# Optimization experiments

Measured on AMD Instinct MI355X. Metric: run time of the kernel, lower is better.

The kernel has to match this reference:

```python
import jax, jax.numpy as jnp
import numpy as np

K = 10
SLOPE = 0.2
FEATS = [3, 64, 128, 256, 512, 1024]
MLP = [1024, 128, 64, 1]
B, N = 8, 2048


def setup_inputs() -> dict:
    key = jax.random.key(0)
    keys = jax.random.split(key, 32)
    inp = {"x": jax.random.normal(keys[0], (B, N, 3), dtype=jnp.float32)}
    ki = 1
    for i in range(5):
        fin, fout = 2 * FEATS[i], FEATS[i + 1]
        s = 1.0 / np.sqrt(fin)
        inp[f"w{i}"] = jax.random.uniform(keys[ki], (fin, fout), jnp.float32, -s, s); ki += 1
        inp[f"b{i}"] = jax.random.uniform(keys[ki], (fout,), jnp.float32, -s, s); ki += 1
    for i in range(3):
        fin, fout = MLP[i], MLP[i + 1]
        s = 1.0 / np.sqrt(fin)
        inp[f"m{i}w"] = jax.random.uniform(keys[ki], (fin, fout), jnp.float32, -s, s); ki += 1
        inp[f"m{i}b"] = jax.random.uniform(keys[ki], (fout,), jnp.float32, -s, s); ki += 1
    return inp


def _knn_idx(xb):
    # xb: [N, F]; squared euclidean distances, self included (dist 0)
    sq = jnp.sum(xb * xb, axis=-1)
    d2 = sq[:, None] + sq[None, :] - 2.0 * (xb @ xb.T)
    _, idx = jax.lax.top_k(-d2, K)  # [N, K] nearest (incl. self)
    return idx


def _edge_conv(x, W, b):
    # x: [B, N, F] -> [B, N, Fout]
    fin = x.shape[-1]
    W1, W2 = W[:fin], W[fin:]  # split concat([x_i, x_j - x_i]) @ W
    idx = jax.vmap(_knn_idx)(x)  # [B, N, K]
    x_j = jax.vmap(lambda xb, ib: xb[ib])(x, idx)  # [B, N, K, F]
    h_center = x @ W1 + b  # [B, N, Fout]
    diff = x_j - x[:, :, None, :]
    h = h_center[:, :, None, :] + jnp.einsum('bnkf,fo->bnko', diff, W2)
    h = jnp.where(h > 0, h, SLOPE * h)  # LeakyReLU(0.2)
    return jnp.max(h, axis=2)  # max aggregation over neighbors


def reference(x, w0, b0, w1, b1, w2, b2, w3, b3, w4, b4,
              m0w, m0b, m1w, m1b, m2w, m2b):
    ws = [(w0, b0), (w1, b1), (w2, b2), (w3, b3), (w4, b4)]
    h = x
    for W, b in ws:
        h = _edge_conv(h, W, b)
    g = jnp.max(h, axis=1)  # MaxPool1d(kernel=2048) -> global max over points: [B, 1024]
    g = g @ m0w + m0b
    g = g @ m1w + m1b
    g = g @ m2w + m2b
    return g  # [B, 1]
```

## Files before the change

kernel.cpp:

```cpp
#include <hip/hip_runtime.h>
#include <hip/hip_bf16.h>
#include <math.h>

#define BB 8
#define NN 2048
#define KK 10
#define BN (BB * NN)
#define HC 1024
#define GCH 64

typedef __attribute__((ext_vector_type(8))) short bf16x8;
typedef __attribute__((ext_vector_type(4))) float f32x4;

__device__ inline unsigned short f2bf(float f) {
    unsigned int u = __float_as_uint(f);
    unsigned int r = u + 0x7fffu + ((u >> 16) & 1u);
    return (unsigned short)(r >> 16);
}
__device__ inline float bf2f(unsigned short h) {
    return __uint_as_float((unsigned int)h << 16);
}

__device__ __forceinline__ void async16(const void* g, void* l) {
    __builtin_amdgcn_global_load_lds(
        (const __attribute__((address_space(1))) void*)g,
        (__attribute__((address_space(3))) void*)l, 16, 0, 0);
}

__global__ void xsplit3_kernel(const float* __restrict__ x,
                               unsigned short* __restrict__ hi,
                               unsigned short* __restrict__ lo,
                               float* __restrict__ sq) {
    int row = blockIdx.x * blockDim.x + threadIdx.x;
    if (row >= BN) return;
    unsigned short hbuf[32], lbuf[32];
#pragma unroll
    for (int f = 0; f < 32; ++f) { hbuf[f] = 0; lbuf[f] = 0; }
    float s = 0.f;
#pragma unroll
    for (int f = 0; f < 3; ++f) {
        float v = x[(size_t)row * 3 + f];
        s += v * v;
        unsigned short h = f2bf(v);
        hbuf[f] = h;
        lbuf[f] = f2bf(v - bf2f(h));
    }
    sq[row] = s;
#pragma unroll
    for (int f = 0; f < 32; f += 8) {
        *(uint4*)&hi[(size_t)row * 32 + f] = *(uint4*)&hbuf[f];
        *(uint4*)&lo[(size_t)row * 32 + f] = *(uint4*)&lbuf[f];
    }
}

__global__ void wsplit_all_kernel(const float* __restrict__ w0, const float* __restrict__ w1,
                                  const float* __restrict__ w2, const float* __restrict__ w3,
                                  const float* __restrict__ w4, unsigned short* __restrict__ WTall) {
    const int fins[5]  = {3, 64, 128, 256, 512};
    const int fpads[5] = {32, 64, 128, 256, 512};
    const int fouts[5] = {64, 128, 256, 512, 1024};
    const int eoff[6]  = {0, 4096, 20480, 86016, 348160, 1396736};
    const int woff[5]  = {0, 8192, 40960, 172032, 696320};
    int i = blockIdx.x * blockDim.x + threadIdx.x;
    if (i >= 1396736) return;
    int l;
    if (i < eoff[1]) l = 0; else if (i < eoff[2]) l = 1;
    else if (i < eoff[3]) l = 2; else if (i < eoff[4]) l = 3; else l = 4;
    int e = i - eoff[l];
    const float* w = (l == 0) ? w0 : (l == 1) ? w1 : (l == 2) ? w2 : (l == 3) ? w3 : w4;
    int fin = fins[l], fpad = fpads[l], fout = fouts[l];
    unsigned short* WT = WTall + woff[l];
    int op = e % (2 * fout);
    int f = e / (2 * fout);
    float v = 0.f;
    if (f < fin) {
        if (op < fout) v = w[(size_t)f * fout + op] - w[(size_t)(fin + f) * fout + op];
        else v = w[(size_t)(fin + f) * fout + (op - fout)];
    }
    unsigned short h = f2bf(v);
    unsigned short lo = f2bf(v - bf2f(h));
    WT[(size_t)op * (2 * fpad) + f] = h;
    WT[(size_t)op * (2 * fpad) + fpad + f] = lo;
}

__global__ __launch_bounds__(256) void knn_gram_kernel(
        const unsigned short* __restrict__ xh, const unsigned short* __restrict__ xl,
        const float* __restrict__ sq, float* __restrict__ d2a,
        float* __restrict__ d2b, int F) {
    int b = blockIdx.y;
    int t = blockIdx.x, ti = 0;
    while (t >= 16 - ti) { t -= 16 - ti; ti++; }
    int tj = ti + t;
    int row0 = ti * 128;
    int col0 = tj * 128;
    const unsigned short* xhb = xh + (size_t)b * NN * F;
    const unsigned short* xlb = xl + (size_t)b * NN * F;
    const float* sqb = sq + (size_t)b * NN;

    __shared__ __align__(16) unsigned char smem_raw[33024];
    unsigned short* Ah = (unsigned short*)smem_raw;
    unsigned short* Al = Ah + 128 * 32;
    unsigned short* Bh = Al + 128 * 32;
    unsigned short* Bl = Bh + 128 * 32;
    float* LT = (float*)smem_raw;

    int tid = threadIdx.x;
    int lane = tid & 63;
    int wave = tid >> 6;
    int wr = (wave >> 1) * 64, wc = (wave & 1) * 64;
    int l15 = lane & 15, kq = lane >> 4;
    int rsub = lane >> 2;
    int csub = (((lane & 3) ^ ((lane >> 3) & 3))) * 8;
    int kqs = (kq ^ ((l15 >> 1) & 3)) * 8;

    f32x4 acc[4][4];
#pragma unroll
    for (int mt = 0; mt < 4; ++mt)
#pragma unroll
        for (int nt = 0; nt < 4; ++nt) acc[mt][nt] = (f32x4){0.f, 0.f, 0.f, 0.f};

    for (int kc = 0; kc < F; kc += 32) {
        __syncthreads();
#pragma unroll
        for (int j = 0; j < 2; ++j) {
            int row = wave * 32 + j * 16 + rsub;
            int dsto = wave * 1024 + j * 512;
            async16(xhb + (size_t)(row0 + row) * F + kc + csub, Ah + dsto);
            async16(xlb + (size_t)(row0 + row) * F + kc + csub, Al + dsto);
            async16(xhb + (size_t)(col0 + row) * F + kc + csub, Bh + dsto);
            async16(xlb + (size_t)(col0 + row) * F + kc + csub, Bl + dsto);
        }
        __syncthreads();
        bf16x8 bh[4], bl[4];
#pragma unroll
        for (int t4 = 0; t4 < 4; ++t4) {
            bh[t4] = *(const bf16x8*)&Bh[(wc + t4 * 16 + l15) * 32 + kqs];
            bl[t4] = *(const bf16x8*)&Bl[(wc + t4 * 16 + l15) * 32 + kqs];
        }
#pragma unroll
        for (int mt = 0; mt < 4; ++mt) {
            bf16x8 ah = *(const bf16x8*)&Ah[(wr + mt * 16 + l15) * 32 + kqs];
            bf16x8 al = *(const bf16x8*)&Al[(wr + mt * 16 + l15) * 32 + kqs];
#pragma unroll
            for (int nt = 0; nt < 4; ++nt) {
                acc[mt][nt] = __builtin_amdgcn_mfma_f32_16x16x32_bf16(ah, bh[nt], acc[mt][nt], 0, 0, 0);
                acc[mt][nt] = __builtin_amdgcn_mfma_f32_16x16x32_bf16(al, bh[nt], acc[mt][nt], 0, 0, 0);
                acc[mt][nt] = __builtin_amdgcn_mfma_f32_16x16x32_bf16(ah, bl[nt], acc[mt][nt], 0, 0, 0);
            }
        }
    }
    {
        float* dst = (col0 < HC) ? d2a : d2b;
        int lc0 = col0 & (HC - 1);
#pragma unroll
        for (int mt = 0; mt < 4; ++mt) {
            int rbase = row0 + wr + mt * 16 + kq * 4;
#pragma unroll
            for (int nt = 0; nt < 4; ++nt) {
                int cc = wc + nt * 16 + l15;
                float sqc = sqb[col0 + cc];
#pragma unroll
                for (int r = 0; r < 4; ++r) {
                    float v = (sqb[rbase + r] + sqc) - 2.f * acc[mt][nt][r];
                    acc[mt][nt][r] = v;
                    dst[((size_t)b * NN + rbase + r) * HC + lc0 + cc] = v;
                }
            }
        }
    }
    if (ti != tj) {
        float* mdst = (row0 < HC) ? d2a : d2b;
        int mc0 = row0 & (HC - 1);
#pragma unroll
        for (int h = 0; h < 2; ++h) {
            __syncthreads();
            if ((wave & 1) == h) {
#pragma unroll
                for (int mt = 0; mt < 4; ++mt)
#pragma unroll
                    for (int nt = 0; nt < 4; ++nt)
#pragma unroll
                        for (int r = 0; r < 4; ++r)
                            LT[(nt * 16 + l15) * 129 + (wr + mt * 16 + kq * 4 + r)] =
                                acc[mt][nt][r];
            }
            __syncthreads();
#pragma unroll
            for (int it = 0; it < 8; ++it) {
                int v = tid + it * 256;
                int lr = v >> 5, c4 = v & 31;
                float4 val;
                val.x = LT[lr * 129 + c4 * 4];
                val.y = LT[lr * 129 + c4 * 4 + 1];
                val.z = LT[lr * 129 + c4 * 4 + 2];
                val.w = LT[lr * 129 + c4 * 4 + 3];
                *(float4*)&mdst[((size_t)b * NN + col0 + h * 64 + lr) * HC + mc0 + c4 * 4] = val;
            }
        }
    }
}

__global__ __launch_bounds__(256) void knn_select_kernel(
        const float* __restrict__ d2a, const float* __restrict__ d2b,
        int* __restrict__ idx) {
    int row = blockIdx.x * 4 + (threadIdx.x >> 6);
    int lane = threadIdx.x & 63;
    const float* ra = d2a + (size_t)row * HC;
    const float* rb = d2b + (size_t)row * HC;

    float4 v[8];
#pragma unroll
    for (int it = 0; it < 4; ++it) {
        v[it]     = *(const float4*)&ra[it * 256 + lane * 4];
        v[it + 4] = *(const float4*)&rb[it * 256 + lane * 4];
    }

    float bestd[KK];
    int besti[KK];
#pragma unroll
    for (int k = 0; k < KK; ++k) { bestd[k] = INFINITY; besti[k] = 0x7fffffff; }

#pragma unroll
    for (int it = 0; it < 8; ++it) {
        int cbase = ((it < 4) ? (it * 256) : (HC + (it - 4) * 256)) + lane * 4;
        float dv[4] = {v[it].x, v[it].y, v[it].z, v[it].w};
#pragma unroll
        for (int s4 = 0; s4 < 4; ++s4) {
            float d = dv[s4];
            if (d < bestd[KK - 1]) {
                bestd[KK - 1] = d;
                besti[KK - 1] = cbase + s4;
#pragma unroll
                for (int s = KK - 1; s > 0; --s) {
                    if (bestd[s] < bestd[s - 1]) {
                        float td = bestd[s]; bestd[s] = bestd[s - 1]; bestd[s - 1] = td;
                        int ti = besti[s]; besti[s] = besti[s - 1]; besti[s - 1] = ti;
                    }
                }
            }
        }
    }

    int h = 0;
    int mywin = 0;
    for (int s = 0; s < KK; ++s) {
        float dd = (h < KK) ? bestd[h] : INFINITY;
        int ii = (h < KK) ? besti[h] : 0x7fffffff;
        float d0 = dd; int i0 = ii;
#pragma unroll
        for (int off = 32; off > 0; off >>= 1) {
            float od = __shfl_xor(dd, off);
            int oi = __shfl_xor(ii, off);
            if (od < dd || (od == dd && oi < ii)) { dd = od; ii = oi; }
        }
        if (lane == s) mywin = ii;
        if (h < KK && i0 == ii && d0 == dd) h++;
    }
    if (lane < KK) idx[(size_t)row * KK + lane] = mywin;
}

__global__ __launch_bounds__(256) void gemm2_mfma_kernel(
        const unsigned short* __restrict__ XSh, const unsigned short* __restrict__ XSl,
        const unsigned short* __restrict__ WT, const float* __restrict__ bias,
        float* __restrict__ Aout, float* __restrict__ Tout, int fin, int fout) {
    int m0 = blockIdx.x * 128;
    int n0 = blockIdx.y * 128;
    __shared__ __align__(16) unsigned short AsB[4 * 128 * 32];
    unsigned short* Ah = AsB;
    unsigned short* Al = Ah + 128 * 32;
    unsigned short* Bh = Al + 128 * 32;
    unsigned short* Bl = Bh + 128 * 32;

    int tid = threadIdx.x;
    int lane = tid & 63;
    int wave = tid >> 6;
    int wr = (wave >> 1) * 64, wc = (wave & 1) * 64;
    int l15 = lane & 15, kq = lane >> 4;
    int rsub = lane >> 2;
    int csub = (((lane & 3) ^ ((lane >> 3) & 3))) * 8;
    int kqs = (kq ^ ((l15 >> 1) & 3)) * 8;
    int w2f = 2 * fin;

    f32x4 acc[4][4];
#pragma unroll
    for (int mt = 0; mt < 4; ++mt)
#pragma unroll
        for (int nt = 0; nt < 4; ++nt) acc[mt][nt] = (f32x4){0.f, 0.f, 0.f, 0.f};

    for (int kc = 0; kc < fin; kc += 32) {
        __syncthreads();
#pragma unroll
        for (int j = 0; j < 2; ++j) {
            int row = wave * 32 + j * 16 + rsub;
            int dsto = wave * 1024 + j * 512;
            async16(XSh + (size_t)(m0 + row) * fin + kc + csub, Ah + dsto);
            async16(XSl + (size_t)(m0 + row) * fin + kc + csub, Al + dsto);
            async16(WT + (size_t)(n0 + row) * w2f + kc + csub, Bh + dsto);
            async16(WT + (size_t)(n0 + row) * w2f + fin + kc + csub, Bl + dsto);
        }
        __syncthreads();
        bf16x8 bh[4], bl[4];
#pragma unroll
        for (int t = 0; t < 4; ++t) {
            bh[t] = *(const bf16x8*)&Bh[(wc + t * 16 + l15) * 32 + kqs];
            bl[t] = *(const bf16x8*)&Bl[(wc + t * 16 + l15) * 32 + kqs];
        }
#pragma unroll
        for (int mt = 0; mt < 4; ++mt) {
            bf16x8 ah = *(const bf16x8*)&Ah[(wr + mt * 16 + l15) * 32 + kqs];
            bf16x8 al = *(const bf16x8*)&Al[(wr + mt * 16 + l15) * 32 + kqs];
#pragma unroll
            for (int nt = 0; nt < 4; ++nt) {
                acc[mt][nt] = __builtin_amdgcn_mfma_f32_16x16x32_bf16(ah, bh[nt], acc[mt][nt], 0, 0, 0);
                acc[mt][nt] = __builtin_amdgcn_mfma_f32_16x16x32_bf16(al, bh[nt], acc[mt][nt], 0, 0, 0);
                acc[mt][nt] = __builtin_amdgcn_mfma_f32_16x16x32_bf16(ah, bl[nt], acc[mt][nt], 0, 0, 0);
            }
        }
    }
#pragma unroll
    for (int mt = 0; mt < 4; ++mt) {
        int mbase = m0 + wr + mt * 16 + kq * 4;
#pragma unroll
        for (int nt = 0; nt < 4; ++nt) {
            int oc = n0 + wc + nt * 16 + l15;
            f32x4 c = acc[mt][nt];
            if (oc < fout) {
                float bv = bias[oc];
#pragma unroll
                for (int r = 0; r < 4; ++r)
                    Aout[(size_t)(mbase + r) * fout + oc] = c[r] + bv;
            } else {
                int o2 = oc - fout;
#pragma unroll
                for (int r = 0; r < 4; ++r)
                    Tout[(size_t)(mbase + r) * fout + o2] = c[r];
            }
        }
    }
}

__global__ __launch_bounds__(256) void gathermax_fused_kernel(
        const float* __restrict__ A, const float* __restrict__ T,
        const int* __restrict__ idx, unsigned short* __restrict__ hi,
        unsigned short* __restrict__ lo, float* __restrict__ sq, int shift) {
    int b = blockIdx.y;
    int wave = threadIdx.x >> 6;
    int lane = threadIdx.x & 63;
    int pnl = blockIdx.x * 4 + wave;
    int pn = (b << 11) + pnl;
    int fout = 1 << shift;
    int nf4 = fout >> 2;
    const float* Tb = T + ((size_t)b << 11) * fout;
    const int* ip = idx + (size_t)pn * KK;
    int j[KK];
#pragma unroll
    for (int k = 0; k < KK; ++k) j[k] = ip[k];

    float s = 0.f;
    for (int f4 = lane; f4 < nf4; f4 += 64) {
        int o = f4 * 4;
        float4 m = {-INFINITY, -INFINITY, -INFINITY, -INFINITY};
#pragma unroll
        for (int k = 0; k < KK; ++k) {
            float4 t = *(const float4*)&Tb[(size_t)j[k] * fout + o];
            m.x = fmaxf(m.x, t.x); m.y = fmaxf(m.y, t.y);
            m.z = fmaxf(m.z, t.z); m.w = fmaxf(m.w, t.w);
        }
        float4 a = *(const float4*)&A[(size_t)pn * fout + o];
        float h4[4];
        h4[0] = a.x + m.x; h4[1] = a.y + m.y; h4[2] = a.z + m.z; h4[3] = a.w + m.w;
        uint2 uh, ul;
        unsigned short hs[4], ls[4];
#pragma unroll
        for (int q = 0; q < 4; ++q) {
            float h = h4[q] > 0.f ? h4[q] : 0.2f * h4[q];
            s += h * h;
            unsigned short hh = f2bf(h);
            hs[q] = hh;
            ls[q] = f2bf(h - bf2f(hh));
        }
        uh.x = (unsigned)hs[0] | ((unsigned)hs[1] << 16);
        uh.y = (unsigned)hs[2] | ((unsigned)hs[3] << 16);
        ul.x = (unsigned)ls[0] | ((unsigned)ls[1] << 16);
        ul.y = (unsigned)ls[2] | ((unsigned)ls[3] << 16);
        *(uint2*)&hi[(size_t)pn * fout + o] = uh;
        *(uint2*)&lo[(size_t)pn * fout + o] = ul;
    }
#pragma unroll
    for (int off = 32; off > 0; off >>= 1) s += __shfl_down(s, off);
    if (lane == 0) sq[pn] = s;
}

__global__ __launch_bounds__(256) void gathermax_gmax_kernel(
        const float* __restrict__ A, const float* __restrict__ T,
        const int* __restrict__ idx, float* __restrict__ gp) {
    int chunk = blockIdx.x;
    int b = blockIdx.y;
    int o = threadIdx.x * 4;
    const float* Tb = T + ((size_t)b << 11) * 1024;
    float4 gm = {-INFINITY, -INFINITY, -INFINITY, -INFINITY};
    for (int p = 0; p < NN / GCH; ++p) {
        int pnl = chunk * (NN / GCH) + p;
        int pn = (b << 11) + pnl;
        const int* ip = idx + (size_t)pn * KK;
        float4 m = {-INFINITY, -INFINITY, -INFINITY, -INFINITY};
#pragma unroll
        for (int k = 0; k < KK; ++k) {
            int j = ip[k];
            float4 t = *(const float4*)&Tb[(size_t)j * 1024 + o];
            m.x = fmaxf(m.x, t.x); m.y = fmaxf(m.y, t.y);
            m.z = fmaxf(m.z, t.z); m.w = fmaxf(m.w, t.w);
        }
        float4 a = *(const float4*)&A[(size_t)pn * 1024 + o];
        float4 h;
        h.x = a.x + m.x; h.y = a.y + m.y; h.z = a.z + m.z; h.w = a.w + m.w;
        h.x = h.x > 0.f ? h.x : 0.2f * h.x;
        h.y = h.y > 0.f ? h.y : 0.2f * h.y;
        h.z = h.z > 0.f ? h.z : 0.2f * h.z;
        h.w = h.w > 0.f ? h.w : 0.2f * h.w;
        gm.x = fmaxf(gm.x, h.x); gm.y = fmaxf(gm.y, h.y);
        gm.z = fmaxf(gm.z, h.z); gm.w = fmaxf(gm.w, h.w);
    }
    *(float4*)&gp[((size_t)chunk * BB + b) * 1024 + o] = gm;
}

__global__ void gmax2_kernel(const float* __restrict__ gp, float* __restrict__ g) {
    int i = blockIdx.x * 256 + threadIdx.x;
    int b = i >> 10, o = i & 1023;
    float m = -INFINITY;
    for (int c = 0; c < GCH; ++c) m = fmaxf(m, gp[((size_t)c * BB + b) * 1024 + o]);
    g[(size_t)b * 1024 + o] = m;
}

__global__ __launch_bounds__(256) void mlp1_kernel(
        const float* __restrict__ g, const float* __restrict__ m0w,
        const float* __restrict__ m0b, float* __restrict__ H1) {
    int wid = blockIdx.x * 4 + (threadIdx.x >> 6);
    int lane = threadIdx.x & 63;
    int b = wid >> 7, t = wid & 127;
    float s = 0.f;
    for (int f = lane; f < 1024; f += 64)
        s += g[(size_t)b * 1024 + f] * m0w[(size_t)f * 128 + t];
#pragma unroll
    for (int off = 32; off > 0; off >>= 1) s += __shfl_down(s, off);
    if (lane == 0) H1[(size_t)b * 128 + t] = s + m0b[t];
}

__global__ __launch_bounds__(256) void mlp2_kernel(
        const float* __restrict__ H1, const float* __restrict__ m1w,
        const float* __restrict__ m1b, float* __restrict__ H2) {
    int wid = blockIdx.x * 4 + (threadIdx.x >> 6);
    int lane = threadIdx.x & 63;
    int b = wid >> 6, t = wid & 63;
    float s = 0.f;
    for (int f = lane; f < 128; f += 64)
        s += H1[(size_t)b * 128 + f] * m1w[(size_t)f * 64 + t];
#pragma unroll
    for (int off = 32; off > 0; off >>= 1) s += __shfl_down(s, off);
    if (lane == 0) H2[(size_t)b * 64 + t] = s + m1b[t];
}

__global__ __launch_bounds__(256) void mlp3_kernel(
        const float* __restrict__ H2, const float* __restrict__ m2w,
        const float* __restrict__ m2b, float* __restrict__ out) {
    int b = blockIdx.x * 4 + (threadIdx.x >> 6);
    int lane = threadIdx.x & 63;
    if (b >= BB) return;
    float s = H2[(size_t)b * 64 + lane] * m2w[lane];
#pragma unroll
    for (int off = 32; off > 0; off >>= 1) s += __shfl_down(s, off);
    if (lane == 0) out[b] = s + m2b[0];
}

extern "C" void kernel_launch(void* const* d_in, const int* in_sizes, int n_in,
                              void* d_out, int out_size, void* d_ws, size_t ws_size,
                              hipStream_t stream) {
    const float* x0 = (const float*)d_in[0];
    const float* w[5], * bi[5];
    for (int i = 0; i < 5; ++i) { w[i] = (const float*)d_in[1 + 2 * i]; bi[i] = (const float*)d_in[2 + 2 * i]; }
    const float* m0w = (const float*)d_in[11]; const float* m0b = (const float*)d_in[12];
    const float* m1w = (const float*)d_in[13]; const float* m1b = (const float*)d_in[14];
    const float* m2w = (const float*)d_in[15]; const float* m2b = (const float*)d_in[16];

    const int fouts[5] = {64, 128, 256, 512, 1024};
    const int shifts[5] = {6, 7, 8, 9, 10};
    const int woff[5] = {0, 8192, 40960, 172032, 696320};
    const size_t WTALL = 2793472;

    float* X0 = (float*)d_ws;
    float* X1 = X0 + (size_t)BN * 1024;
    float* T  = X1 + (size_t)BN * 1024;
    float* SQ = T  + (size_t)BN * 1024;
    int*   IDX = (int*)(SQ + BN);
    unsigned short* XSh = (unsigned short*)(IDX + (size_t)BN * KK);
    unsigned short* XSl = XSh + (size_t)BN * 512;
    unsigned short* WTall = XSl + (size_t)BN * 512;
    float* GP = (float*)(WTall + WTALL);
    float* G  = GP + (size_t)GCH * BB * 1024;
    float* H1 = G + (size_t)BB * 1024;
    float* H2 = H1 + (size_t)BB * 128;
    float* bufs[2] = {X0, X1};

    xsplit3_kernel<<<(BN + 255) / 256, 256, 0, stream>>>(x0, XSh, XSl, SQ);
    wsplit_all_kernel<<<(1396736 + 255) / 256, 256, 0, stream>>>(w[0], w[1], w[2], w[3], w[4], WTall);

    int fin = 3;
    for (int l = 0; l < 5; ++l) {
        int fout = fouts[l];
        float* nxt = bufs[l & 1];
        int Fg = (l == 0) ? 32 : fin;

        dim3 gg2(136, BB);
        knn_gram_kernel<<<gg2, 256, 0, stream>>>(XSh, XSl, SQ, T, nxt, Fg);
        knn_select_kernel<<<BN / 4, 256, 0, stream>>>(T, nxt, IDX);

        dim3 gg(BN / 128, (2 * fout) / 128);
        gemm2_mfma_kernel<<<gg, 256, 0, stream>>>(XSh, XSl, WTall + woff[l], bi[l], nxt, T, Fg, fout);

        if (l < 4) {
            dim3 gmg(NN / 4, BB);
            gathermax_fused_kernel<<<gmg, 256, 0, stream>>>(nxt, T, IDX, XSh, XSl, SQ, shifts[l]);
        } else {
            dim3 gmg(GCH, BB);
            gathermax_gmax_kernel<<<gmg, 256, 0, stream>>>(nxt, T, IDX, GP);
        }

        fin = fout;
    }

    gmax2_kernel<<<32, 256, 0, stream>>>(GP, G);
    mlp1_kernel<<<256, 256, 0, stream>>>(G, m0w, m0b, H1);
    mlp2_kernel<<<128, 256, 0, stream>>>(H1, m1w, m1b, H2);
    mlp3_kernel<<<2, 256, 0, stream>>>(H2, m2w, m2b, (float*)d_out);
}
```

Before: 1.031 ms.

## Add 256x256-tile 8-wave phased MFMA GEMM for deeper edge-conv layers

Measured after the change: 1.002 ms. 2.8% less time.

```diff
diff --git a/kernel.cpp b/kernel.cpp
--- a/kernel.cpp
+++ b/kernel.cpp
@@ -339,6 +339,190 @@
     }
 }
 
+__device__ __forceinline__ const unsigned short* tbaseA(
+        const unsigned short* XSh, const unsigned short* XSl, int F, int t) {
+    int ko = t * 64;
+    if (ko < F) return XSh + ko;
+    if (ko < 2 * F) return XSl + (ko - F);
+    return XSh + (ko - 2 * F);
+}
+__device__ __forceinline__ const unsigned short* tbaseB(
+        const unsigned short* WT, int F, int t) {
+    int ko = t * 64;
+    if (ko < F) return WT + ko;
+    if (ko < 2 * F) return WT + (ko - F);
+    return WT + F + (ko - 2 * F);
+}
+
+#define GBAR() asm volatile("s_barrier" ::: "memory")
+
+__global__ __launch_bounds__(512, 2) void gemm2_8ph_kernel(
+        const unsigned short* __restrict__ XSh, const unsigned short* __restrict__ XSl,
+        const unsigned short* __restrict__ WT, const float* __restrict__ bias,
+        float* __restrict__ Aout, float* __restrict__ Tout, int F, int fout, int nby) {
+    __shared__ __align__(16) unsigned short Lds[65536];
+
+    int nwg = gridDim.x;
+    int bid = blockIdx.x;
+    int q = nwg >> 3;
+    int swz = (bid & 7) * q + (bid >> 3);
+    int by = swz % nby;
+    int bx = swz / nby;
+    int m0 = bx * 256, n0 = by * 256;
+
+    int tid = threadIdx.x;
+    int lane = tid & 63;
+    int wave = tid >> 6;
+    int mw = wave >> 2;
+    int nw = wave & 3;
+    int l15 = lane & 15, kq = lane >> 4;
+    int rx7 = l15 & 7;
+
+    int isA = (wave < 4);
+    size_t rowmul = isA ? (size_t)F : (size_t)(2 * F);
+    int orgn = isA ? m0 : n0;
+    int r8 = lane >> 3;
+    int cb8 = ((lane & 7) ^ r8) * 8;
+    int subb = (wave & 3) * 8;
+    int ldsoA = isA ? 0 : 16384;
+
+    int nt = (3 * F) >> 6;
+
+    f32x4 acc[8][4];
+#pragma unroll
+    for (int mt = 0; mt < 8; ++mt)
+#pragma unroll
+        for (int nn = 0; nn < 4; ++nn) acc[mt][nn] = (f32x4){0.f, 0.f, 0.f, 0.f};
+
+    auto stage = [&](const unsigned short* tb, int par, int j) {
+        int sub = subb + j;
+        async16(tb + (size_t)(orgn + sub * 8 + r8) * rowmul + cb8,
+                Lds + par * 32768 + ldsoA + sub * 512);
+    };
+
+    {
+        const unsigned short* t0 = isA ? tbaseA(XSh, XSl, F, 0) : tbaseB(WT, F, 0);
+        const unsigned short* t1 = isA ? tbaseA(XSh, XSl, F, 1) : tbaseB(WT, F, 1);
+#pragma unroll
+        for (int j = 0; j < 8; ++j) stage(t0, 0, j);
+#pragma unroll
+        for (int j = 0; j < 4; ++j) stage(t1, 1, j);
+    }
+    asm volatile("s_waitcnt vmcnt(4)" ::: "memory");
+    GBAR();
+
+    for (int t = 0; t < nt; ++t) {
+        const unsigned short* Ab = Lds + (t & 1) * 32768;
+        const unsigned short* Bb = Ab + 16384;
+        bool s1 = (t + 1 < nt), s2 = (t + 2 < nt);
+        const unsigned short* tb1 = s1 ? (isA ? tbaseA(XSh, XSl, F, t + 1)
+                                              : tbaseB(WT, F, t + 1)) : XSh;
+        const unsigned short* tb2 = s2 ? (isA ? tbaseA(XSh, XSl, F, t + 2)
+                                              : tbaseB(WT, F, t + 2)) : XSh;
+        int p1 = (t + 1) & 1, p0 = t & 1;
+
+        bf16x8 aF[4][2], bA[2][2], bB[2][2];
+
+#pragma unroll
+        for (int mt = 0; mt < 4; ++mt)
+#pragma unroll
+            for (int kf = 0; kf < 2; ++kf)
+                aF[mt][kf] = *(const bf16x8*)&Ab[(mw * 128 + mt * 16 + l15) * 64 +
+                                                 ((kf * 4 + kq) ^ rx7) * 8];
+#pragma unroll
+        for (int nn = 0; nn < 2; ++nn)
+#pragma unroll
+            for (int kf = 0; kf < 2; ++kf)
+                bA[nn][kf] = *(const bf16x8*)&Bb[(nw * 64 + nn * 16 + l15) * 64 +
+                                                 ((kf * 4 + kq) ^ rx7) * 8];
+        if (s1) { stage(tb1, p1, 4); stage(tb1, p1, 5); }
+        GBAR();
+        __builtin_amdgcn_s_setprio(1);
+#pragma unroll
+        for (int mt = 0; mt < 4; ++mt)
+#pragma unroll
+            for (int nn = 0; nn < 2; ++nn) {
+                acc[mt][nn] = __builtin_amdgcn_mfma_f32_16x16x32_bf16(aF[mt][0], bA[nn][0], acc[mt][nn], 0, 0, 0);
+                acc[mt][nn] = __builtin_amdgcn_mfma_f32_16x16x32_bf16(aF[mt][1], bA[nn][1], acc[mt][nn], 0, 0, 0);
+            }
+        __builtin_amdgcn_s_setprio(0);
+        GBAR();
+
+#pragma unroll
+        for (int nn = 0; nn < 2; ++nn)
+#pragma unroll
+            for (int kf = 0; kf < 2; ++kf)
+                bB[nn][kf] = *(const bf16x8*)&Bb[(nw * 64 + (nn + 2) * 16 + l15) * 64 +
+                                                 ((kf * 4 + kq) ^ rx7) * 8];
+        if (s1) { stage(tb1, p1, 6); stage(tb1, p1, 7); }
+        GBAR();
+        __builtin_amdgcn_s_setprio(1);
+#pragma unroll
+        for (int mt = 0; mt < 4; ++mt)
+#pragma unroll
+            for (int nn = 0; nn < 2; ++nn) {
+                acc[mt][nn + 2] = __builtin_amdgcn_mfma_f32_16x16x32_bf16(aF[mt][0], bB[nn][0], acc[mt][nn + 2], 0, 0, 0);
+                acc[mt][nn + 2] = __builtin_amdgcn_mfma_f32_16x16x32_bf16(aF[mt][1], bB[nn][1], acc[mt][nn + 2], 0, 0, 0);
+            }
+        __builtin_amdgcn_s_setprio(0);
+        GBAR();
+
+#pragma unroll
+        for (int mt = 0; mt < 4; ++mt)
+#pragma unroll
+            for (int kf = 0; kf < 2; ++kf)
+                aF[mt][kf] = *(const bf16x8*)&Ab[(mw * 128 + (mt + 4) * 16 + l15) * 64 +
+                                                 ((kf * 4 + kq) ^ rx7) * 8];
+        GBAR();
+        __builtin_amdgcn_s_setprio(1);
+#pragma unroll
+        for (int mt = 0; mt < 4; ++mt)
+#pragma unroll
+            for (int nn = 0; nn < 2; ++nn) {
+                acc[mt + 4][nn] = __builtin_amdgcn_mfma_f32_16x16x32_bf16(aF[mt][0], bA[nn][0], acc[mt + 4][nn], 0, 0, 0);
+                acc[mt + 4][nn] = __builtin_amdgcn_mfma_f32_16x16x32_bf16(aF[mt][1], bA[nn][1], acc[mt + 4][nn], 0, 0, 0);
+            }
+        __builtin_amdgcn_s_setprio(0);
+        GBAR();
+
+        if (s2) { stage(tb2, p0, 0); stage(tb2, p0, 1); stage(tb2, p0, 2); stage(tb2, p0, 3); }
+        GBAR();
+        __builtin_amdgcn_s_setprio(1);
+#pragma unroll
+        for (int mt = 0; mt < 4; ++mt)
+#pragma unroll
+            for (int nn = 0; nn < 2; ++nn) {
+                acc[mt + 4][nn + 2] = __builtin_amdgcn_mfma_f32_16x16x32_bf16(aF[mt][0], bB[nn][0], acc[mt + 4][nn + 2], 0, 0, 0);
+                acc[mt + 4][nn + 2] = __builtin_amdgcn_mfma_f32_16x16x32_bf16(aF[mt][1], bB[nn][1], acc[mt + 4][nn + 2], 0, 0, 0);
+            }
+        __builtin_amdgcn_s_setprio(0);
+        if (s2)      asm volatile("s_waitcnt vmcnt(4)" ::: "memory");
+        else if (s1) asm volatile("s_waitcnt vmcnt(0)" ::: "memory");
+        GBAR();
+    }
+
+#pragma unroll
+    for (int mt = 0; mt < 8; ++mt) {
+        int mbase = m0 + mw * 128 + mt * 16 + kq * 4;
+#pragma unroll
+        for (int nn = 0; nn < 4; ++nn) {
+            int oc = n0 + nw * 64 + nn * 16 + l15;
+            f32x4 c = acc[mt][nn];
+            if (oc < fout) {
+                float bv = bias[oc];
+#pragma unroll
+                for (int r = 0; r < 4; ++r)
+                    Aout[(size_t)(mbase + r) * fout + oc] = c[r] + bv;
+            } else {
+                int o2 = oc - fout;
+#pragma unroll
+                for (int r = 0; r < 4; ++r)
+                    Tout[(size_t)(mbase + r) * fout + o2] = c[r];
+            }
+        }
+    }
+}
+
 __global__ __launch_bounds__(256) void gathermax_fused_kernel(
         const float* __restrict__ A, const float* __restrict__ T,
         const int* __restrict__ idx, unsigned short* __restrict__ hi,
@@ -514,8 +698,14 @@
         knn_gram_kernel<<<gg2, 256, 0, stream>>>(XSh, XSl, SQ, T, nxt, Fg);
         knn_select_kernel<<<BN / 4, 256, 0, stream>>>(T, nxt, IDX);
 
-        dim3 gg(BN / 128, (2 * fout) / 128);
-        gemm2_mfma_kernel<<<gg, 256, 0, stream>>>(XSh, XSl, WTall + woff[l], bi[l], nxt, T, Fg, fout);
+        if (l >= 2) {
+            int nby = (2 * fout) / 256;
+            gemm2_8ph_kernel<<<dim3(64 * nby), 512, 0, stream>>>(
+                XSh, XSl, WTall + woff[l], bi[l], nxt, T, fin, fout, nby);
+        } else {
+            dim3 gg(BN / 128, (2 * fout) / 128);
+            gemm2_mfma_kernel<<<gg, 256, 0, stream>>>(XSh, XSl, WTall + woff[l], bi[l], nxt, T, Fg, fout);
+        }
 
         if (l < 4) {
             dim3 gmg(NN / 4, BB);
```

## Co-schedule kNN top-k selection with projection GEMM in one interleaved launch

Applied to the files above, without the earlier changes.

Result: slower. 1.187 ms (+15.1%).

```diff
diff --git a/kernel.cpp b/kernel.cpp
--- a/kernel.cpp
+++ b/kernel.cpp
@@ -8,6 +8,7 @@
 #define BN (BB * NN)
 #define HC 1024
 #define GCH 64
+#define NSEL (BN / 4)
 
 typedef __attribute__((ext_vector_type(8))) short bf16x8;
 typedef __attribute__((ext_vector_type(4))) float f32x4;
@@ -200,11 +201,9 @@
     }
 }
 
-__global__ __launch_bounds__(256) void knn_select_kernel(
+__device__ __forceinline__ void select_body(
         const float* __restrict__ d2a, const float* __restrict__ d2b,
-        int* __restrict__ idx) {
-    int row = blockIdx.x * 4 + (threadIdx.x >> 6);
-    int lane = threadIdx.x & 63;
+        int* __restrict__ idx, int row, int lane) {
     const float* ra = d2a + (size_t)row * HC;
     const float* rb = d2b + (size_t)row * HC;
 
@@ -259,19 +258,17 @@
     if (lane < KK) idx[(size_t)row * KK + lane] = mywin;
 }
 
-__global__ __launch_bounds__(256) void gemm2_mfma_kernel(
+__device__ __forceinline__ void gemm_body(
         const unsigned short* __restrict__ XSh, const unsigned short* __restrict__ XSl,
         const unsigned short* __restrict__ WT, const float* __restrict__ bias,
-        float* __restrict__ Aout, float* __restrict__ Tout, int fin, int fout) {
-    int m0 = blockIdx.x * 128;
-    int n0 = blockIdx.y * 128;
+        float* __restrict__ Aout, float* __restrict__ Tout, int fin, int fout,
+        int m0, int n0, int tid) {
     __shared__ __align__(16) unsigned short AsB[4 * 128 * 32];
     unsigned short* Ah = AsB;
     unsigned short* Al = Ah + 128 * 32;
     unsigned short* Bh = Al + 128 * 32;
     unsigned short* Bl = Bh + 128 * 32;
 
-    int tid = threadIdx.x;
     int lane = tid & 63;
     int wave = tid >> 6;
     int wr = (wave >> 1) * 64, wc = (wave & 1) * 64;
@@ -336,6 +333,29 @@
                     Tout[(size_t)(mbase + r) * fout + o2] = c[r];
             }
         }
+    }
+}
+
+__global__ __launch_bounds__(256) void gemm_sel_kernel(
+        const unsigned short* __restrict__ XSh, const unsigned short* __restrict__ XSl,
+        const unsigned short* __restrict__ WT, const float* __restrict__ bias,
+        float* __restrict__ Aout, float* __restrict__ Tout, int fin, int fout,
+        int n0base, int ngemm, int nmb,
+        const float* __restrict__ d2a, const float* __restrict__ d2b,
+        int* __restrict__ idx, int nsel) {
+    int i = blockIdx.x;
+    int total = ngemm + nsel;
+    int sb = (int)((long long)i * nsel / total);
+    bool is_sel = ((long long)(i + 1) * nsel / total) > sb;
+    int tid = threadIdx.x;
+    if (is_sel) {
+        int row = sb * 4 + (tid >> 6);
+        select_body(d2a, d2b, idx, row, tid & 63);
+    } else {
+        int g = i - sb;
+        int m0 = (g % nmb) * 128;
+        int n0 = n0base + (g / nmb) * 128;
+        gemm_body(XSh, XSl, WT, bias, Aout, Tout, fin, fout, m0, n0, tid);
     }
 }
 
@@ -487,42 +507,74 @@
     const int woff[5] = {0, 8192, 40960, 172032, 696320};
     const size_t WTALL = 2793472;
 
-    float* X0 = (float*)d_ws;
-    float* X1 = X0 + (size_t)BN * 1024;
-    float* T  = X1 + (size_t)BN * 1024;
-    float* SQ = T  + (size_t)BN * 1024;
-    int*   IDX = (int*)(SQ + BN);
-    unsigned short* XSh = (unsigned short*)(IDX + (size_t)BN * KK);
-    unsigned short* XSl = XSh + (size_t)BN * 512;
-    unsigned short* WTall = XSl + (size_t)BN * 512;
-    float* GP = (float*)(WTall + WTALL);
-    float* G  = GP + (size_t)GCH * BB * 1024;
-    float* H1 = G + (size_t)BB * 1024;
-    float* H2 = H1 + (size_t)BB * 128;
+    size_t fbuf = (size_t)BN * 1024;
+    size_t rest_bytes = (size_t)BN * 4 + (size_t)BN * KK * 4
+                      + (size_t)BN * 512 * 2 * 2 + WTALL * 2
+                      + (size_t)GCH * BB * 1024 * 4 + (size_t)BB * 1024 * 4
+                      + (size_t)BB * 128 * 4 + (size_t)BB * 64 * 4;
+    bool full = ws_size >= 4 * fbuf * 4 + rest_bytes;
+
+    char* p = (char*)d_ws;
+    float* X0 = (float*)p; p += fbuf * 4;
+    float* X1 = (float*)p; p += fbuf * 4;
+    float* T  = (float*)p; p += fbuf * 4;
+    float* X2 = nullptr;
+    if (full) { X2 = (float*)p; p += fbuf * 4; }
+    float* SQ = (float*)p; p += (size_t)BN * 4;
+    int*   IDX = (int*)p;  p += (size_t)BN * KK * 4;
+    unsigned short* XSh = (unsigned short*)p; p += (size_t)BN * 512 * 2;
+    unsigned short* XSl = (unsigned short*)p; p += (size_t)BN * 512 * 2;
+    unsigned short* WTall = (unsigned short*)p; p += WTALL * 2;
+    float* GP = (float*)p; p += (size_t)GCH * BB * 1024 * 4;
+    float* G  = (float*)p; p += (size_t)BB * 1024 * 4;
+    float* H1 = (float*)p; p += (size_t)BB * 128 * 4;
+    float* H2 = (float*)p;
     float* bufs[2] = {X0, X1};
 
     xsplit3_kernel<<<(BN + 255) / 256, 256, 0, stream>>>(x0, XSh, XSl, SQ);
     wsplit_all_kernel<<<(1396736 + 255) / 256, 256, 0, stream>>>(w[0], w[1], w[2], w[3], w[4], WTall);
 
     int fin = 3;
+    int nmb = BN / 128;
     for (int l = 0; l < 5; ++l) {
         int fout = fouts[l];
-        float* nxt = bufs[l & 1];
+        float* Ab = bufs[l & 1];
+        float* Db = bufs[(l + 1) & 1];
         int Fg = (l == 0) ? 32 : fin;
+        const unsigned short* WTl = WTall + woff[l];
 
         dim3 gg2(136, BB);
-        knn_gram_kernel<<<gg2, 256, 0, stream>>>(XSh, XSl, SQ, T, nxt, Fg);
-        knn_select_kernel<<<BN / 4, 256, 0, stream>>>(T, nxt, IDX);
-
-        dim3 gg(BN / 128, (2 * fout) / 128);
-        gemm2_mfma_kernel<<<gg, 256, 0, stream>>>(XSh, XSl, WTall + woff[l], bi[l], nxt, T, Fg, fout);
-
+        knn_gram_kernel<<<gg2, 256, 0, stream>>>(XSh, XSl, SQ, T, Db, Fg);
+
+        if (full) {
+            int ngemm = nmb * ((2 * fout) / 128);
+            gemm_sel_kernel<<<ngemm + NSEL, 256, 0, stream>>>(
+                XSh, XSl, WTl, bi[l], Ab, X2, Fg, fout, 0, ngemm, nmb,
+                T, Db, IDX, NSEL);
+        } else if (fout >= 128) {
+            int ng1 = nmb * (fout / 128);
+            gemm_sel_kernel<<<ng1 + NSEL, 256, 0, stream>>>(
+                XSh, XSl, WTl, bi[l], Ab, T, Fg, fout, 0, ng1, nmb,
+                T, Db, IDX, NSEL);
+            gemm_sel_kernel<<<ng1, 256, 0, stream>>>(
+                XSh, XSl, WTl, bi[l], Ab, T, Fg, fout, fout, ng1, nmb,
+                T, Db, IDX, 0);
+        } else {
+            gemm_sel_kernel<<<NSEL, 256, 0, stream>>>(
+                XSh, XSl, WTl, bi[l], Ab, T, Fg, fout, 0, 0, nmb,
+                T, Db, IDX, NSEL);
+            gemm_sel_kernel<<<nmb, 256, 0, stream>>>(
+                XSh, XSl, WTl, bi[l], Ab, T, Fg, fout, 0, nmb, nmb,
+                T, Db, IDX, 0);
+        }
+
+        float* Tp = full ? X2 : T;
         if (l < 4) {
             dim3 gmg(NN / 4, BB);
-            gathermax_fused_kernel<<<gmg, 256, 0, stream>>>(nxt, T, IDX, XSh, XSl, SQ, shifts[l]);
+            gathermax_fused_kernel<<<gmg, 256, 0, stream>>>(Ab, Tp, IDX, XSh, XSl, SQ, shifts[l]);
         } else {
             dim3 gmg(GCH, BB);
-            gathermax_gmax_kernel<<<gmg, 256, 0, stream>>>(nxt, T, IDX, GP);
+            gathermax_gmax_kernel<<<gmg, 256, 0, stream>>>(Ab, Tp, IDX, GP);
         }
 
         fin = fout;
```
